# Kernel tuning notes

Measured on AMD Instinct MI355X. Metric: run time of the kernel, lower is better.

## Reference

```python
import jax, jax.numpy as jnp
import numpy as np

D_EMBED, N_HEADS, D_HEAD = 1024, 16, 64
B, S = 2, 2048


def setup_inputs() -> dict:
    key = jax.random.key(0)
    ks = jax.random.split(key, 5)
    sc = 0.02
    return {
        "x": jax.random.normal(ks[0], (B, S, D_EMBED), dtype=jnp.float32),
        "w_q": jax.random.normal(ks[1], (D_EMBED, N_HEADS * D_HEAD), dtype=jnp.float32) * sc,
        "w_k": jax.random.normal(ks[2], (D_EMBED, N_HEADS * D_HEAD), dtype=jnp.float32) * sc,
        "w_v": jax.random.normal(ks[3], (D_EMBED, N_HEADS * D_HEAD), dtype=jnp.float32) * sc,
        "w_o": jax.random.normal(ks[4], (N_HEADS * D_HEAD, D_EMBED), dtype=jnp.float32) * sc,
    }


def reference(x, w_q, w_k, w_v, w_o):
    b, s, _ = x.shape
    # projections -> [b, h, s, d]
    def proj(w):
        return jnp.einsum('bse,ef->bsf', x, w).reshape(b, s, N_HEADS, D_HEAD).transpose(0, 2, 1, 3)
    q, k, v = proj(w_q), proj(w_k), proj(w_v)
    scores = jnp.einsum('bhqd,bhkd->bhqk', q, k) / jnp.sqrt(jnp.float32(D_HEAD))
    causal = jnp.tril(jnp.ones((s, s), dtype=bool))  # True where allowed
    scores = jnp.where(causal[None, None], scores, -jnp.inf)
    attn = jax.nn.softmax(scores, axis=-1)
    out = jnp.einsum('bhqk,bhkd->bhqd', attn, v)
    out = out.transpose(0, 2, 1, 3).reshape(b, s, N_HEADS * D_HEAD)
    return jnp.einsum('bsf,fe->bse', out, w_o)
```

## Files before the change

kernel.cpp:

```cpp
#include <hip/hip_runtime.h>
#include <hip/hip_bf16.h>
#include <cstdint>
#include <cstddef>


#define B_  2
#define S_  2048
#define E_  1024
#define NH_ 16
#define DH_ 64
#define M_  (B_*S_)
#define F_  (NH_*DH_)

typedef unsigned short u16;
typedef short short8 __attribute__((ext_vector_type(8)));
typedef float f32x4  __attribute__((ext_vector_type(4)));

__device__ __forceinline__ float bf2f(u16 u) {
    union { unsigned int i; float f; } c; c.i = ((unsigned int)u) << 16; return c.f;
}
__device__ __forceinline__ u16 f2bf(float f) {
    union { float f; unsigned int i; } c; c.f = f;
    unsigned int x = c.i;
    x += 0x7fffu + ((x >> 16) & 1u);
    return (u16)(x >> 16);
}

__global__ __launch_bounds__(256)
void xconv(const float* __restrict__ x, u16* __restrict__ xb)
{
    size_t i = (size_t)blockIdx.x * 256 + threadIdx.x;
    const float4* s = (const float4*)(x + i*8);
    float4 a = s[0], b = s[1];
    short8 o;
    ((u16*)&o)[0] = f2bf(a.x); ((u16*)&o)[1] = f2bf(a.y);
    ((u16*)&o)[2] = f2bf(a.z); ((u16*)&o)[3] = f2bf(a.w);
    ((u16*)&o)[4] = f2bf(b.x); ((u16*)&o)[5] = f2bf(b.y);
    ((u16*)&o)[6] = f2bf(b.z); ((u16*)&o)[7] = f2bf(b.w);
    ((short8*)xb)[i] = o;
}

__global__ __launch_bounds__(256)
void wtrans(const float* __restrict__ W, u16* __restrict__ Wt)
{
    __shared__ u16 t[64][66];
    const int tid = threadIdx.x;
    const int n0 = blockIdx.x * 64;
    const int k0 = blockIdx.y * 64;

    {
        int kk = tid >> 2, nseg = (tid & 3) * 16;
        const float4* src = (const float4*)(W + (size_t)(k0+kk)*F_ + n0 + nseg);
        #pragma unroll
        for (int v = 0; v < 4; ++v) {
            float4 u = src[v];
            t[kk][nseg + v*4 + 0] = f2bf(u.x);
            t[kk][nseg + v*4 + 1] = f2bf(u.y);
            t[kk][nseg + v*4 + 2] = f2bf(u.z);
            t[kk][nseg + v*4 + 3] = f2bf(u.w);
        }
    }
    __syncthreads();
    {
        int nn = tid >> 2, kseg = (tid & 3) * 16;
        short8 o0, o1;
        #pragma unroll
        for (int i = 0; i < 8; ++i) ((u16*)&o0)[i] = t[kseg + i][nn];
        #pragma unroll
        for (int i = 0; i < 8; ++i) ((u16*)&o1)[i] = t[kseg + 8 + i][nn];
        u16* dst = Wt + (size_t)(n0+nn)*E_ + k0 + kseg;
        ((short8*)dst)[0] = o0;
        ((short8*)dst)[1] = o1;
    }
}

template<int MODE>
__global__ __launch_bounds__(256)
void gemm_bf16(const u16* __restrict__ A, const u16* __restrict__ Wt,
               void* __restrict__ Out0, void* __restrict__ Out1,
               void* __restrict__ Out2)
{
    __shared__ __align__(16) char lds[32768];
    char* lA = lds;
    char* lB = lds + 16384;

    const int tid  = threadIdx.x;
    const int lane = tid & 63;
    const int w    = tid >> 6;
    const int wr   = w >> 1, wc = w & 1;
    const int g    = lane >> 4;
    const int q15  = lane & 15;
    const int bx   = blockIdx.x;
    const int by   = blockIdx.y;
    const int z    = (MODE == 0) ? blockIdx.z : 0;

    const u16* Wz  = Wt + (size_t)z * E_ * F_;
    void*      Out = (z == 0) ? Out0 : (z == 1) ? Out1 : Out2;

    const int lr  = lane >> 3;
    const int lc  = lane & 7;
    const int swz = ((lc ^ lr) << 4);

    const int b2 = by >> 4;
    const int s0 = (by & 15) * 128;

    f32x4 acc[4][4];
    #pragma unroll
    for (int i = 0; i < 4; ++i)
        #pragma unroll
        for (int j = 0; j < 4; ++j) acc[i][j] = (f32x4){0.f,0.f,0.f,0.f};

    for (int it = 0; it < E_/64; ++it) {
        const int k0 = it * 64;
        __syncthreads();
        #pragma unroll
        for (int i = 0; i < 4; ++i) {
            const int row = w*32 + i*8 + lr;
            const char* ga;
            if (MODE == 0) {
                ga = (const char*)A + (size_t)(by*128 + row)*2048 + k0*2 + swz;
            } else {
                const int h = k0 >> 6;
                ga = (const char*)A +
                     ((size_t)(b2*NH_ + h)*S_ + s0 + row)*128 + swz;
            }
            __builtin_amdgcn_global_load_lds(
                (const unsigned int*)ga,
                (unsigned int*)(lA + w*4096 + i*1024), 16, 0, 0);
        }
        #pragma unroll
        for (int i = 0; i < 4; ++i) {
            const int row = w*32 + i*8 + lr;
            const char* gb = (const char*)Wz + (size_t)(bx*128 + row)*2048
                             + k0*2 + swz;
            __builtin_amdgcn_global_load_lds(
                (const unsigned int*)gb,
                (unsigned int*)(lB + w*4096 + i*1024), 16, 0, 0);
        }
        __syncthreads();

        #pragma unroll
        for (int s = 0; s < 2; ++s) {
            short8 af[4], bfr[4];
            #pragma unroll
            for (int mt = 0; mt < 4; ++mt) {
                int row = wr*64 + mt*16 + q15;
                af[mt] = *(const short8*)(lA + row*128 + ((s*64 + 16*g) ^ ((row&7)<<4)));
            }
            #pragma unroll
            for (int nt = 0; nt < 4; ++nt) {
                int n = wc*64 + nt*16 + q15;
                bfr[nt] = *(const short8*)(lB + n*128 + ((s*64 + 16*g) ^ ((n&7)<<4)));
            }
            #pragma unroll
            for (int mt = 0; mt < 4; ++mt)
                #pragma unroll
                for (int nt = 0; nt < 4; ++nt)
                    acc[mt][nt] = __builtin_amdgcn_mfma_f32_16x16x32_bf16(
                        af[mt], bfr[nt], acc[mt][nt], 0, 0, 0);
        }
    }

    #pragma unroll
    for (int mt = 0; mt < 4; ++mt) {
        #pragma unroll
        for (int r = 0; r < 4; ++r) {
            int grow = by*128 + wr*64 + mt*16 + 4*g + r;
            if (MODE == 0) {
                int bb = grow >> 11, ss = grow & (S_-1);
                #pragma unroll
                for (int nt = 0; nt < 4; ++nt) {
                    int n = bx*128 + wc*64 + nt*16 + q15;
                    int hh = n >> 6, dd = n & 63;
                    ((u16*)Out)[(((size_t)bb*NH_ + hh)*S_ + ss)*DH_ + dd] =
                        f2bf(acc[mt][nt][r]);
                }
            } else {
                #pragma unroll
                for (int nt = 0; nt < 4; ++nt) {
                    int n = bx*128 + wc*64 + nt*16 + q15;
                    ((float*)Out)[(size_t)grow * F_ + n] = acc[mt][nt][r];
                }
            }
        }
    }
}

__global__ __launch_bounds__(256)
void vtrans(const u16* __restrict__ V, u16* __restrict__ Vt)
{
    __shared__ u16 t[64][66];
    const int tid = threadIdx.x;
    const int st  = blockIdx.x;
    const int bh  = blockIdx.y;

    {
        int s = tid >> 2, dseg = (tid & 3) * 16;
        const u16* src = V + ((size_t)bh*S_ + st*64 + s)*DH_ + dseg;
        short8 a = ((const short8*)src)[0];
        short8 b = ((const short8*)src)[1];
        *(short8*)&t[s][dseg]     = a;
        *(short8*)&t[s][dseg + 8] = b;
    }
    __syncthreads();
    {
        int d = tid >> 2, sseg = (tid & 3) * 16;
        short8 o0, o1;
        #pragma unroll
        for (int i = 0; i < 8; ++i) ((u16*)&o0)[i] = t[sseg + i][d];
        #pragma unroll
        for (int i = 0; i < 8; ++i) ((u16*)&o1)[i] = t[sseg + 8 + i][d];
        u16* dst = Vt + ((size_t)bh*DH_ + d)*S_ + st*64 + sseg;
        ((short8*)dst)[0] = o0;
        ((short8*)dst)[1] = o1;
    }
}

__global__ __launch_bounds__(256)
void attn_v7(const u16* Q, const u16* __restrict__ K,
             const u16* __restrict__ Vt, u16* O)
{
    __shared__ __align__(16) char vls[2*8192];
    __shared__ __align__(16) char kls[2*8192];
    __shared__ __align__(16) char pls[4][2048];

    const int tid  = threadIdx.x;
    const int lane = tid & 63;
    const int w    = tid >> 6;
    const int g    = lane >> 4;
    const int q15  = lane & 15;

    const int blk = blockIdx.x;
    const int qg  = 31 - (blk >> 5);
    const int bh  = blk & 31;
    const int q0  = qg * 64;

    const u16* Kb  = K  + (size_t)bh * S_ * DH_;
    const u16* Vtb = Vt + (size_t)bh * DH_ * S_;

    short8 qf0, qf1;
    {
        const u16* Qp = Q + ((size_t)bh * S_ + q0 + w*16 + q15) * DH_ + g*8;
        qf0 = *(const short8*)(Qp);
        qf1 = *(const short8*)(Qp + 32);
    }

    f32x4 o[4];
    #pragma unroll
    for (int dt = 0; dt < 4; ++dt) o[dt] = (f32x4){0.f,0.f,0.f,0.f};
    float mrow = -1e30f, lrow = 0.f;

    char* plw = (char*)&pls[w][0];
    const int sd = tid >> 2;
    const int sk = (tid & 3) * 32;

    short8 svv0, svv1, svk0, svk1;
    auto LOADX = [&](int t) {
        const u16* vs = Vtb + (size_t)sd * S_ + t*64 + (sk >> 1);
        svv0 = ((const short8*)vs)[0];
        svv1 = ((const short8*)vs)[1];
        const u16* ks = Kb + (size_t)(t*64 + sd) * DH_ + (sk >> 1);
        svk0 = ((const short8*)ks)[0];
        svk1 = ((const short8*)ks)[1];
    };
    auto WRITEX = [&](int buf) {
        char* vdst = vls + buf*8192 + sd*128;
        *(short8*)(vdst + ((sk     ) ^ ((sd&7)<<4))) = svv0;
        *(short8*)(vdst + ((sk + 16) ^ ((sd&7)<<4))) = svv1;
        char* kdst = kls + buf*8192 + sd*128;
        *(short8*)(kdst + ((sk     ) ^ ((sd&7)<<4))) = svk0;
        *(short8*)(kdst + ((sk + 16) ^ ((sd&7)<<4))) = svk1;
    };

    LOADX(0);
    WRITEX(0);
    __syncthreads();

    for (int kt = 0; ; ++kt) {
        const bool more = (kt < qg);
        if (more) LOADX(kt + 1);

        const char* kt_ = kls + (kt & 1) * 8192;
        const char* vt_ = vls + (kt & 1) * 8192;

        float p[16];
        __builtin_amdgcn_s_setprio(1);
        #pragma unroll
        for (int t = 0; t < 4; ++t) {
            int r = t*16 + q15;
            short8 kf0 = *(const short8*)(kt_ + r*128 + ((16*g     ) ^ ((r&7)<<4)));
            short8 kf1 = *(const short8*)(kt_ + r*128 + ((16*g + 64) ^ ((r&7)<<4)));
            f32x4 st = (f32x4){0.f,0.f,0.f,0.f};
            st = __builtin_amdgcn_mfma_f32_16x16x32_bf16(kf0, qf0, st, 0, 0, 0);
            st = __builtin_amdgcn_mfma_f32_16x16x32_bf16(kf1, qf1, st, 0, 0, 0);
            #pragma unroll
            for (int r2 = 0; r2 < 4; ++r2) p[t*4+r2] = st[r2] * 0.125f;
        }
        __builtin_amdgcn_s_setprio(0);

        if (kt == qg) {
            #pragma unroll
            for (int t = 0; t < 4; ++t)
                #pragma unroll
                for (int r = 0; r < 4; ++r)
                    if (16*t + 4*g + r > w*16 + q15) p[t*4+r] = -1e30f;
        }

        float tmax = p[0];
        #pragma unroll
        for (int i = 1; i < 16; ++i) tmax = fmaxf(tmax, p[i]);
        tmax = fmaxf(tmax, __shfl_xor(tmax, 16));
        tmax = fmaxf(tmax, __shfl_xor(tmax, 32));
        float mnew = fmaxf(mrow, tmax);
        float rsc  = __expf(mrow - mnew);
        mrow = mnew;
        float psum = 0.f;
        #pragma unroll
        for (int i = 0; i < 16; ++i) { p[i] = __expf(p[i] - mnew); psum += p[i]; }
        psum += __shfl_xor(psum, 16);
        psum += __shfl_xor(psum, 32);
        lrow = lrow * rsc + psum;

        #pragma unroll
        for (int r = 0; r < 4; ++r) {
            float rr = __shfl(rsc, 4*g + r);
            #pragma unroll
            for (int dt = 0; dt < 4; ++dt) o[dt][r] *= rr;
        }

        #pragma unroll
        for (int t = 0; t < 4; ++t) {
            unsigned r0, r1;
            asm("v_cvt_pk_bf16_f32 %0, %1, %2"
                : "=v"(r0) : "v"(p[t*4+0]), "v"(p[t*4+1]));
            asm("v_cvt_pk_bf16_f32 %0, %1, %2"
                : "=v"(r1) : "v"(p[t*4+2]), "v"(p[t*4+3]));
            int byte = q15*128 + ((32*t + 8*g) ^ ((q15&7)<<4));
            uint2 pk; pk.x = r0; pk.y = r1;
            *(uint2*)(plw + byte) = pk;
        }

        __builtin_amdgcn_s_setprio(1);
        #pragma unroll
        for (int c = 0; c < 2; ++c) {
            int pb = q15*128 + ((64*c + 16*g) ^ ((q15&7)<<4));
            short8 pf = *(const short8*)(plw + pb);
            #pragma unroll
            for (int dt = 0; dt < 4; ++dt) {
                int d = dt*16 + q15;
                int vb = d*128 + ((64*c + 16*g) ^ ((d&7)<<4));
                short8 vf = *(const short8*)(vt_ + vb);
                o[dt] = __builtin_amdgcn_mfma_f32_16x16x32_bf16(pf, vf, o[dt], 0, 0, 0);
            }
        }
        __builtin_amdgcn_s_setprio(0);

        if (!more) break;
        WRITEX((kt + 1) & 1);
        __syncthreads();
    }

    float inv = 1.f / lrow;
    #pragma unroll
    for (int r = 0; r < 4; ++r) {
        float li = __shfl(inv, 4*g + r);
        int qrow = q0 + w*16 + 4*g + r;
        #pragma unroll
        for (int dt = 0; dt < 4; ++dt) {
            O[((size_t)bh * S_ + qrow) * DH_ + dt*16 + q15] = f2bf(o[dt][r] * li);
        }
    }
}

extern "C" void kernel_launch(void* const* d_in, const int* in_sizes, int n_in,
                              void* d_out, int out_size, void* d_ws, size_t ws_size,
                              hipStream_t stream) {
    (void)in_sizes; (void)n_in; (void)out_size; (void)ws_size;
    const float* x  = (const float*)d_in[0];
    const float* wq = (const float*)d_in[1];
    const float* wk = (const float*)d_in[2];
    const float* wv = (const float*)d_in[3];
    const float* wo = (const float*)d_in[4];

    u16* Qw = (u16*)d_ws;
    u16* Kw = Qw + (size_t)M_ * F_;
    u16* Vw = Kw + (size_t)M_ * F_;

    u16* D0 = (u16*)d_out;
    u16* xb = D0 + (size_t)4*1024*1024;

    xconv<<<dim3(M_*E_/8/256), 256, 0, stream>>>(x, xb);
    wtrans<<<dim3(16,16), 256, 0, stream>>>(wq, D0 + 0*(size_t)E_*F_);
    wtrans<<<dim3(16,16), 256, 0, stream>>>(wk, D0 + 1*(size_t)E_*F_);
    wtrans<<<dim3(16,16), 256, 0, stream>>>(wv, D0 + 2*(size_t)E_*F_);

    gemm_bf16<0><<<dim3(F_/128, M_/128, 3), 256, 0, stream>>>(
        xb, D0, (void*)Qw, (void*)Kw, (void*)Vw);

    vtrans<<<dim3(S_/64, B_*NH_), 256, 0, stream>>>(Vw, D0);
    wtrans<<<dim3(16,16), 256, 0, stream>>>(wo, Vw);

    attn_v7<<<dim3(B_*NH_*(S_/64)), 256, 0, stream>>>(Qw, Kw, D0, Qw);

    gemm_bf16<2><<<dim3(F_/128, M_/128, 1), 256, 0, stream>>>(
        Qw, Vw, d_out, d_out, d_out);
}
```

Baseline: 132.0 us.

## Fold softmax scale into Q, use exp2 with lazy rescale, merge prep kernels

```diff
diff --git a/kernel.cpp b/kernel.cpp
--- a/kernel.cpp
+++ b/kernel.cpp
@@ -16,9 +16,8 @@
 typedef short short8 __attribute__((ext_vector_type(8)));
 typedef float f32x4  __attribute__((ext_vector_type(4)));
 
-__device__ __forceinline__ float bf2f(u16 u) {
-    union { unsigned int i; float f; } c; c.i = ((unsigned int)u) << 16; return c.f;
-}
+#define QSCALE 0.18033688011112042f
+
 __device__ __forceinline__ u16 f2bf(float f) {
     union { float f; unsigned int i; } c; c.f = f;
     unsigned int x = c.i;
@@ -27,17 +26,58 @@
 }
 
 __global__ __launch_bounds__(256)
-void xconv(const float* __restrict__ x, u16* __restrict__ xb)
+void prep(const float* __restrict__ x,
+          const float* __restrict__ wq, const float* __restrict__ wk,
+          const float* __restrict__ wv,
+          u16* __restrict__ xb, u16* __restrict__ Wt)
 {
-    size_t i = (size_t)blockIdx.x * 256 + threadIdx.x;
-    const float4* s = (const float4*)(x + i*8);
-    float4 a = s[0], b = s[1];
-    short8 o;
-    ((u16*)&o)[0] = f2bf(a.x); ((u16*)&o)[1] = f2bf(a.y);
-    ((u16*)&o)[2] = f2bf(a.z); ((u16*)&o)[3] = f2bf(a.w);
-    ((u16*)&o)[4] = f2bf(b.x); ((u16*)&o)[5] = f2bf(b.y);
-    ((u16*)&o)[6] = f2bf(b.z); ((u16*)&o)[7] = f2bf(b.w);
-    ((short8*)xb)[i] = o;
+    const int tid = threadIdx.x;
+    const int b   = blockIdx.x;
+    if (b < 2048) {
+        size_t i = (size_t)b * 256 + tid;
+        const float4* s = (const float4*)(x + i*8);
+        float4 a = s[0], bb = s[1];
+        short8 o;
+        ((u16*)&o)[0] = f2bf(a.x);  ((u16*)&o)[1] = f2bf(a.y);
+        ((u16*)&o)[2] = f2bf(a.z);  ((u16*)&o)[3] = f2bf(a.w);
+        ((u16*)&o)[4] = f2bf(bb.x); ((u16*)&o)[5] = f2bf(bb.y);
+        ((u16*)&o)[6] = f2bf(bb.z); ((u16*)&o)[7] = f2bf(bb.w);
+        ((short8*)xb)[i] = o;
+        return;
+    }
+    __shared__ u16 t[64][66];
+    const int wb = b - 2048;
+    const int wi = wb >> 8;
+    const int tt = wb & 255;
+    const int n0 = (tt & 15) * 64;
+    const int k0 = (tt >> 4) * 64;
+    const float* W = (wi == 0) ? wq : (wi == 1) ? wk : wv;
+    u16* dst0 = Wt + (size_t)wi * E_ * F_;
+
+    {
+        int kk = tid >> 2, nseg = (tid & 3) * 16;
+        const float4* src = (const float4*)(W + (size_t)(k0+kk)*F_ + n0 + nseg);
+        #pragma unroll
+        for (int v = 0; v < 4; ++v) {
+            float4 u = src[v];
+            t[kk][nseg + v*4 + 0] = f2bf(u.x);
+            t[kk][nseg + v*4 + 1] = f2bf(u.y);
+            t[kk][nseg + v*4 + 2] = f2bf(u.z);
+            t[kk][nseg + v*4 + 3] = f2bf(u.w);
+        }
+    }
+    __syncthreads();
+    {
+        int nn = tid >> 2, kseg = (tid & 3) * 16;
+        short8 o0, o1;
+        #pragma unroll
+        for (int i = 0; i < 8; ++i) ((u16*)&o0)[i] = t[kseg + i][nn];
+        #pragma unroll
+        for (int i = 0; i < 8; ++i) ((u16*)&o1)[i] = t[kseg + 8 + i][nn];
+        u16* dst = dst0 + (size_t)(n0+nn)*E_ + k0 + kseg;
+        ((short8*)dst)[0] = o0;
+        ((short8*)dst)[1] = o1;
+    }
 }
 
 __global__ __launch_bounds__(256)
@@ -47,7 +87,6 @@
     const int tid = threadIdx.x;
     const int n0 = blockIdx.x * 64;
     const int k0 = blockIdx.y * 64;
-
     {
         int kk = tid >> 2, nseg = (tid & 3) * 16;
         const float4* src = (const float4*)(W + (size_t)(k0+kk)*F_ + n0 + nseg);
@@ -96,6 +135,7 @@
 
     const u16* Wz  = Wt + (size_t)z * E_ * F_;
     void*      Out = (z == 0) ? Out0 : (z == 1) ? Out1 : Out2;
+    const float osc = (MODE == 0 && z == 0) ? QSCALE : 1.0f;
 
     const int lr  = lane >> 3;
     const int lc  = lane & 7;
@@ -173,7 +213,7 @@
                     int n = bx*128 + wc*64 + nt*16 + q15;
                     int hh = n >> 6, dd = n & 63;
                     ((u16*)Out)[(((size_t)bb*NH_ + hh)*S_ + ss)*DH_ + dd] =
-                        f2bf(acc[mt][nt][r]);
+                        f2bf(acc[mt][nt][r] * osc);
                 }
             } else {
                 #pragma unroll
@@ -217,7 +257,7 @@
 }
 
 __global__ __launch_bounds__(256)
-void attn_v7(const u16* Q, const u16* __restrict__ K,
+void attn_v8(const u16* Q, const u16* __restrict__ K,
              const u16* __restrict__ Vt, u16* O)
 {
     __shared__ __align__(16) char vls[2*8192];
@@ -294,7 +334,7 @@
             st = __builtin_amdgcn_mfma_f32_16x16x32_bf16(kf0, qf0, st, 0, 0, 0);
             st = __builtin_amdgcn_mfma_f32_16x16x32_bf16(kf1, qf1, st, 0, 0, 0);
             #pragma unroll
-            for (int r2 = 0; r2 < 4; ++r2) p[t*4+r2] = st[r2] * 0.125f;
+            for (int r2 = 0; r2 < 4; ++r2) p[t*4+r2] = st[r2];
         }
         __builtin_amdgcn_s_setprio(0);
 
@@ -311,21 +351,30 @@
         for (int i = 1; i < 16; ++i) tmax = fmaxf(tmax, p[i]);
         tmax = fmaxf(tmax, __shfl_xor(tmax, 16));
         tmax = fmaxf(tmax, __shfl_xor(tmax, 32));
-        float mnew = fmaxf(mrow, tmax);
-        float rsc  = __expf(mrow - mnew);
-        mrow = mnew;
-        float psum = 0.f;
-        #pragma unroll
-        for (int i = 0; i < 16; ++i) { p[i] = __expf(p[i] - mnew); psum += p[i]; }
-        psum += __shfl_xor(psum, 16);
-        psum += __shfl_xor(psum, 32);
-        lrow = lrow * rsc + psum;
-
-        #pragma unroll
-        for (int r = 0; r < 4; ++r) {
-            float rr = __shfl(rsc, 4*g + r);
-            #pragma unroll
-            for (int dt = 0; dt < 4; ++dt) o[dt][r] *= rr;
+
+        if (__all(tmax <= mrow + 8.0f)) {
+            float psum = 0.f;
+            #pragma unroll
+            for (int i = 0; i < 16; ++i) { p[i] = exp2f(p[i] - mrow); psum += p[i]; }
+            psum += __shfl_xor(psum, 16);
+            psum += __shfl_xor(psum, 32);
+            lrow += psum;
+        } else {
+            float mnew = fmaxf(mrow, tmax);
+            float rsc  = exp2f(mrow - mnew);
+            mrow = mnew;
+            float psum = 0.f;
+            #pragma unroll
+            for (int i = 0; i < 16; ++i) { p[i] = exp2f(p[i] - mrow); psum += p[i]; }
+            psum += __shfl_xor(psum, 16);
+            psum += __shfl_xor(psum, 32);
+            lrow = lrow * rsc + psum;
+            #pragma unroll
+            for (int r = 0; r < 4; ++r) {
+                float rr = __shfl(rsc, 4*g + r);
+                #pragma unroll
+                for (int dt = 0; dt < 4; ++dt) o[dt][r] *= rr;
+            }
         }
 
         #pragma unroll
@@ -389,10 +438,7 @@
     u16* D0 = (u16*)d_out;
     u16* xb = D0 + (size_t)4*1024*1024;
 
-    xconv<<<dim3(M_*E_/8/256), 256, 0, stream>>>(x, xb);
-    wtrans<<<dim3(16,16), 256, 0, stream>>>(wq, D0 + 0*(size_t)E_*F_);
-    wtrans<<<dim3(16,16), 256, 0, stream>>>(wk, D0 + 1*(size_t)E_*F_);
-    wtrans<<<dim3(16,16), 256, 0, stream>>>(wv, D0 + 2*(size_t)E_*F_);
+    prep<<<dim3(2048 + 768), 256, 0, stream>>>(x, wq, wk, wv, xb, D0);
 
     gemm_bf16<0><<<dim3(F_/128, M_/128, 3), 256, 0, stream>>>(
         xb, D0, (void*)Qw, (void*)Kw, (void*)Vw);
@@ -400,7 +446,7 @@
     vtrans<<<dim3(S_/64, B_*NH_), 256, 0, stream>>>(Vw, D0);
     wtrans<<<dim3(16,16), 256, 0, stream>>>(wo, Vw);
 
-    attn_v7<<<dim3(B_*NH_*(S_/64)), 256, 0, stream>>>(Qw, Kw, D0, Qw);
+    attn_v8<<<dim3(B_*NH_*(S_/64)), 256, 0, stream>>>(Qw, Kw, D0, Qw);
 
     gemm_bf16<2><<<dim3(F_/128, M_/128, 1), 256, 0, stream>>>(
         Qw, Vw, d_out, d_out, d_out);
```

New measurement: 139.6 us. 1.06x slower.
